# Kernel tuning notes

Hardware: AMD Instinct MI355X
Metric: run time of the kernel (lower is better)

The kernel has to match this reference:

```python
import jax, jax.numpy as jnp
import numpy as np

H = 32
W = 32
HIDDEN = 64
NUM_CLASSES = 10
BATCH = 128


def setup_inputs() -> dict:
    key = jax.random.key(0)
    ks = jax.random.split(key, 5)
    D = 4 * HIDDEN * H * W  # number_of_output_dimensions()
    return {
        "x": jax.random.normal(ks[0], (BATCH, 1, H, W), jnp.float32),
        "w_in": jax.random.normal(ks[1], (HIDDEN, 1), jnp.float32) * 0.1,
        "b_in": jnp.zeros((HIDDEN,), jnp.float32),
        "w_state": jax.random.normal(ks[2], (HIDDEN, HIDDEN, 2), jnp.float32) * (1.0 / np.sqrt(2 * HIDDEN)),
        "b_state": jnp.zeros((HIDDEN,), jnp.float32),
        "w_fc": jax.random.normal(ks[3], (D, NUM_CLASSES), jnp.float32) * 0.01,
        "b_fc": jnp.zeros((NUM_CLASSES,), jnp.float32),
    }


def _skew(x):
    # x: [B,1,H,W] -> [B,1,H,W+H-1]; row r shifted right by r (diagonal skew)
    Ws = W + H - 1
    col = jnp.arange(Ws)[None, :] - jnp.arange(H)[:, None]  # [H,Ws]
    valid = ((col >= 0) & (col < W)).astype(x.dtype)
    colc = jnp.clip(col, 0, W - 1)
    rows = jnp.arange(H)[:, None]
    return x[:, :, rows, colc] * valid[None, None]


def _one_direction(x, w_in, b_in, w_state, b_state):
    # Diagonal-scan MDRNN over skewed columns.
    B = x.shape[0]
    xs = _skew(x)  # [B,1,H,Ws]
    # Input projection for all columns at once (1x1 conv equivalent)
    xin = jnp.einsum('oc,bchw->bohw', w_in, xs) + b_in[None, :, None, None]
    cols = jnp.moveaxis(xin, 3, 0)  # [Ws,B,HIDDEN,H]

    w_up, w_same = w_state[:, :, 0], w_state[:, :, 1]

    def step(h, xc):
        # conv1d(kernel=2, padding=1) over column, bottom padding removed:
        # out[r] = w_up @ h[r-1] + w_same @ h[r]
        h_up = jnp.pad(h, ((0, 0), (0, 0), (1, 0)))[:, :, :H]
        s = (jnp.einsum('oi,bir->bor', w_up, h_up)
             + jnp.einsum('oi,bir->bor', w_same, h)
             + b_state[None, :, None])
        hn = jnp.tanh(s + xc)
        return hn, hn

    h0 = jnp.zeros((B, HIDDEN, H), x.dtype)
    _, ys = jax.lax.scan(step, h0, cols)  # [Ws,B,HIDDEN,H]
    acts = jnp.moveaxis(ys, 0, 3)  # [B,HIDDEN,H,Ws]
    # Unskew: out[..., r, c] = acts[..., r, c + r]
    ccols = jnp.arange(W)[None, :] + jnp.arange(H)[:, None]  # [H,W]
    rows = jnp.arange(H)[:, None]
    return acts[:, :, rows, ccols]  # [B,HIDDEN,H,W]


def reference(x, w_in, b_in, w_state, b_state, w_fc, b_fc):
    B = x.shape[0]
    # Four scanning directions via flips on dims 2 and 3, concatenated on batch
    x2 = x[:, :, ::-1, :]
    x3 = x[:, :, :, ::-1]
    x4 = x[:, :, ::-1, ::-1]
    xm = jnp.concatenate([x, x2, x3, x4], axis=0)  # [4B,1,H,W]
    acts = _one_direction(xm, w_in, b_in, w_state, b_state)  # [4B,HIDDEN,H,W]
    # index_select interleaving: example b gets its 4 direction copies contiguously
    sel = (jnp.arange(B)[:, None] + B * jnp.arange(4)[None, :]).reshape(-1)
    a = acts[sel].reshape(B, -1)  # [B, 4*HIDDEN*H*W]
    logits = a @ w_fc + b_fc
    return jax.nn.log_softmax(logits, axis=-1)
```

## Files before the change

### kernel.cpp

```cpp
#include <hip/hip_runtime.h>
#include <hip/hip_bf16.h>

#define NHID 64
#define NT   63
#define NBD  512
#define HLDS_STR 72
#define XSTR 35

typedef __attribute__((ext_vector_type(8))) short bf16x8;
typedef __attribute__((ext_vector_type(4))) float f32x4;

__device__ __forceinline__ float tanh_fast(float x) {
    const float e = __expf(2.0f * x);
    const float r = __builtin_amdgcn_rcpf(e + 1.0f);
    return 1.0f - 2.0f * r;
}

__device__ __forceinline__ unsigned int cvt_pk_bf16(float lo, float hi) {
    unsigned int r;
    asm("v_cvt_pk_bf16_f32 %0, %1, %2" : "=v"(r) : "v"(lo), "v"(hi));
    return r;
}

__device__ __forceinline__ float bf2f(unsigned int u16) {
    return __uint_as_float(u16 << 16);
}

#define SKEW_R0(t)  ((t) > 31 ? (t) - 31 : 0)
#define SKEW_R1(t)  ((t) < 31 ? (t) : 31)
#define SKEW_OFF(t) ((t) < 32 ? ((t) * ((t) + 1)) >> 1 : 1024 - (((63 - (t)) * (64 - (t))) >> 1))

#define LGKM_BARRIER() do {                                   \
    asm volatile("s_waitcnt lgkmcnt(0)" ::: "memory");        \
    __builtin_amdgcn_s_barrier();                             \
    asm volatile("" ::: "memory");                            \
} while (0)

__global__ __launch_bounds__(256, 2) void k_main(
    const float* __restrict__ x,
    const float* __restrict__ w_in,
    const float* __restrict__ b_in,
    const float* __restrict__ w_state,
    const float* __restrict__ b_state,
    unsigned short* __restrict__ acts_c,
    const float* __restrict__ w_fc,
    unsigned short* __restrict__ wt_swz)
{
    __shared__ __align__(16) unsigned short hA0[33 * HLDS_STR];
    __shared__ __align__(16) unsigned short hA1[33 * HLDS_STR];
    __shared__ __align__(16) unsigned short hB0[33 * HLDS_STR];
    __shared__ __align__(16) unsigned short hB1[33 * HLDS_STR];
    __shared__ float xsA[32 * XSTR];
    __shared__ float xsB[32 * XSTR];

    const int tid = threadIdx.x;

    if (blockIdx.x >= 256) {
        const int rel = blockIdx.x - 256;
        const int t   = rel >> 6;
        const int sub = rel & 63;
        const int r0 = SKEW_R0(t), r1 = SKEW_R1(t);
        const int cnt = r1 - r0 + 1;
        const int span = cnt << 10;
        int f = sub * 2048 + tid * 8;
        const int fdst = f;
        if (f >= 4 * span) return;
        int d = 0;
        while (f >= span) { f -= span; ++d; }
        const int ks   = f >> 9;
        const int lane = (f >> 3) & 63;
        const int g = lane >> 4, n = lane & 15;
        unsigned int pk[4];
        #pragma unroll
        for (int jj = 0; jj < 4; ++jj) {
            float v[2] = {0.0f, 0.0f};
            #pragma unroll
            for (int h = 0; h < 2; ++h) {
                const int j = jj * 2 + h;
                const int k = ks * 32 + g * 8 + j;
                const int r = r0 + (k >> 6);
                const int o = k & 63;
                const int c = t - r;
                if (n < 10)
                    v[h] = w_fc[((((size_t)(d * 64 + o)) << 10) + (r << 5) + c) * 10 + n];
            }
            pk[jj] = cvt_pk_bf16(v[0], v[1]);
        }
        uint4 st; st.x = pk[0]; st.y = pk[1]; st.z = pk[2]; st.w = pk[3];
        *(uint4*)(wt_swz + (size_t)SKEW_OFF(t) * 4096 + fdst) = st;
        return;
    }

    const int blk = blockIdx.x;
    const int bdA = 2 * blk;
    const int bdB = 2 * blk + 1;
    const int d   = bdA >> 7;
    const int bA  = bdA & 127;
    const int lane = tid & 63;
    const int wave = tid >> 6;
    const int wp = wave & 1;
    const int nt = wave >> 1;
    const int n  = lane & 15;
    const int g  = lane >> 4;

    const bool flr = (d & 1) != 0;
    const bool flc = (d & 2) != 0;
    const float* xbA = x + (size_t)bA * 1024;
    for (int idx = tid; idx < 1024; idx += 256) {
        const int r = idx >> 5, c = idx & 31;
        const int src = (flr ? 31 - r : r) * 32 + (flc ? 31 - c : c);
        xsA[r * XSTR + c] = xbA[src];
        xsB[r * XSTR + c] = xbA[1024 + src];
    }

    for (int m2 = tid; m2 < (33 * HLDS_STR) / 2; m2 += 256) {
        ((unsigned int*)hA0)[m2] = 0u;
        ((unsigned int*)hA1)[m2] = 0u;
        ((unsigned int*)hB0)[m2] = 0u;
        ((unsigned int*)hB1)[m2] = 0u;
    }

    bf16x8 a0[4], a1[4];
    #pragma unroll
    for (int wl = 0; wl < 2; ++wl) {
        const int o = wp * 32 + wl * 16 + n;
        #pragma unroll
        for (int kt = 0; kt < 4; ++kt) {
            const int s  = kt >> 1;
            const int cb = (kt & 1) * 32 + g * 8;
            bf16x8 w8;
            #pragma unroll
            for (int j = 0; j < 8; ++j) {
                const float w = w_state[((size_t)o * 64 + cb + j) * 2 + s];
                w8[j] = (short)(cvt_pk_bf16(w, 0.0f) & 0xffffu);
            }
            if (wl == 0) a0[kt] = w8; else a1[kt] = w8;
        }
    }

    float biasr[2][4], winr[2][4];
    #pragma unroll
    for (int wl = 0; wl < 2; ++wl)
        #pragma unroll
        for (int j = 0; j < 4; ++j) {
            const int o = wp * 32 + wl * 16 + g * 4 + j;
            biasr[wl][j] = b_in[o] + b_state[o];
            winr[wl][j]  = w_in[o];
        }

    const int r_out = nt * 16 + n;
    const int rdoff = r_out * HLDS_STR + g * 8;
    const int wroff = (r_out + 1) * HLDS_STR;
    const int cb0 = wp * 32 + g * 4;
    const int tlo = nt * 16;
    const float* xsA_r = &xsA[r_out * XSTR];
    const float* xsB_r = &xsB[r_out * XSTR];

    unsigned short* actpA = acts_c + (size_t)bdA * 65536 + (size_t)r_out * 1984 + cb0;
    unsigned short* actpB = acts_c + (size_t)bdB * 65536 + (size_t)r_out * 1984 + cb0;

    __syncthreads();

#define MFMA(F, B, C) C = __builtin_amdgcn_mfma_f32_16x16x32_bf16(F, B, C, 0, 0, 0)
#define EPI(WL, SA, SB, XV, WBUF, ACTP) {                                        \
    const float h0 = tanh_fast(SA[0] + SB[0] + biasr[WL][0] + winr[WL][0] * (XV)); \
    const float h1 = tanh_fast(SA[1] + SB[1] + biasr[WL][1] + winr[WL][1] * (XV)); \
    const float h2 = tanh_fast(SA[2] + SB[2] + biasr[WL][2] + winr[WL][2] * (XV)); \
    const float h3 = tanh_fast(SA[3] + SB[3] + biasr[WL][3] + winr[WL][3] * (XV)); \
    uint2 pk; pk.x = cvt_pk_bf16(h0, h1); pk.y = cvt_pk_bf16(h2, h3);            \
    *(uint2*)&WBUF[wroff + cb0 + (WL) * 16] = pk;                                \
    if (stv) *(uint2*)((ACTP) + (WL) * 16) = pk;                                 \
}

#define STEP(T, RA_, WA_, RB_, WB_) do {                                         \
    if ((unsigned)((T) - tlo) < 48u) {                                           \
        const bf16x8 fA0 = *(const bf16x8*)&RA_[rdoff];                          \
        const bf16x8 fA1 = *(const bf16x8*)&RA_[rdoff + 32];                     \
        const bf16x8 fA2 = *(const bf16x8*)&RA_[rdoff + HLDS_STR];               \
        const bf16x8 fA3 = *(const bf16x8*)&RA_[rdoff + HLDS_STR + 32];          \
        const bf16x8 fB0 = *(const bf16x8*)&RB_[rdoff];                          \
        const bf16x8 fB1 = *(const bf16x8*)&RB_[rdoff + 32];                     \
        const bf16x8 fB2 = *(const bf16x8*)&RB_[rdoff + HLDS_STR];               \
        const bf16x8 fB3 = *(const bf16x8*)&RB_[rdoff + HLDS_STR + 32];          \
        f32x4 sA0a = {0,0,0,0}, sA0b = {0,0,0,0};                                \
        f32x4 sA1a = {0,0,0,0}, sA1b = {0,0,0,0};                                \
        f32x4 sB0a = {0,0,0,0}, sB0b = {0,0,0,0};                                \
        f32x4 sB1a = {0,0,0,0}, sB1b = {0,0,0,0};                                \
        MFMA(a0[0], fA0, sA0a); MFMA(a1[0], fA0, sA1a);                          \
        MFMA(a0[0], fB0, sB0a); MFMA(a1[0], fB0, sB1a);                          \
        MFMA(a0[2], fA2, sA0b); MFMA(a1[2], fA2, sA1b);                          \
        MFMA(a0[2], fB2, sB0b); MFMA(a1[2], fB2, sB1b);                          \
        MFMA(a0[1], fA1, sA0a); MFMA(a1[1], fA1, sA1a);                          \
        MFMA(a0[1], fB1, sB0a); MFMA(a1[1], fB1, sB1a);                          \
        MFMA(a0[3], fA3, sA0b); MFMA(a1[3], fA3, sA1b);                          \
        MFMA(a0[3], fB3, sB0b); MFMA(a1[3], fB3, sB1b);                          \
        const int c_ = (T) - r_out;                                              \
        const bool stv = (unsigned)c_ < 32u;                                     \
        const float xvA = stv ? xsA_r[c_ & 31] : 0.0f;                           \
        const float xvB = stv ? xsB_r[c_ & 31] : 0.0f;                           \
        EPI(0, sA0a, sA0b, xvA, WA_, actpA); EPI(1, sA1a, sA1b, xvA, WA_, actpA);\
        EPI(0, sB0a, sB0b, xvB, WB_, actpB); EPI(1, sB1a, sB1b, xvB, WB_, actpB);\
    }                                                                            \
    LGKM_BARRIER();                                                              \
    actpA += 64; actpB += 64;                                                    \
} while (0)

    for (int sp = 0; sp < 31; ++sp) {
        const int t = 2 * sp;
        STEP(t,     hA0, hA1, hB0, hB1);
        STEP(t + 1, hA1, hA0, hB1, hB0);
    }
    STEP(62, hA0, hA1, hB0, hB1);
#undef STEP
#undef EPI
#undef MFMA
}

__global__ __launch_bounds__(256, 4) void k_fc(
    const unsigned short* __restrict__ acts_c,
    const unsigned short* __restrict__ wt_swz,
    float* __restrict__ partial)
{
    const int tid = threadIdx.x;
    const int blk = blockIdx.x;
    const int t   = blk >> 3;
    const int d   = (blk >> 1) & 3;
    const int mh  = blk & 1;
    const int lane = tid & 63;
    const int wv  = tid >> 6;
    const int g   = lane >> 4;
    const int n   = lane & 15;

    const int r0 = SKEW_R0(t), r1 = SKEW_R1(t);
    const int cnt = r1 - r0 + 1;
    const int off = SKEW_OFF(t);

    const int tb = d * 128 + mh * 64 + wv * 16;
    const unsigned short* Ap = acts_c + (size_t)(tb + n) * 65536
                             + (size_t)r0 * 1984 + (size_t)t * 64 + g * 8;
    const unsigned short* Bp = wt_swz
        + ((size_t)off * 4 + (size_t)d * cnt) * 1024 + lane * 8;

    f32x4 acc = {0.f, 0.f, 0.f, 0.f};
    #pragma unroll 2
    for (int q = 0; q < cnt; ++q) {
        const bf16x8 a0  = *(const bf16x8*)(Ap);
        const bf16x8 bb0 = *(const bf16x8*)(Bp);
        const bf16x8 a1  = *(const bf16x8*)(Ap + 32);
        const bf16x8 bb1 = *(const bf16x8*)(Bp + 512);
        acc = __builtin_amdgcn_mfma_f32_16x16x32_bf16(a0, bb0, acc, 0, 0, 0);
        acc = __builtin_amdgcn_mfma_f32_16x16x32_bf16(a1, bb1, acc, 0, 0, 0);
        Ap += 1984;
        Bp += 1024;
    }
    const int batch = tb + g * 4;
    #pragma unroll
    for (int reg = 0; reg < 4; ++reg)
        partial[((size_t)t * 512 + batch + reg) * 16 + n] = acc[reg];
}

__global__ __launch_bounds__(256) void k_out(
    const float* __restrict__ partial,
    const float* __restrict__ b_fc,
    float* __restrict__ out)
{
    __shared__ float lred[252 * 10];
    __shared__ float lgs[10];
    __shared__ float lse;
    const int b = blockIdx.x;
    const int tid = threadIdx.x;
    if (tid < 252) {
        const int t = tid >> 2, d = tid & 3;
        const float* p = partial + ((size_t)t * 512 + d * 128 + b) * 16;
        #pragma unroll
        for (int n2 = 0; n2 < 10; ++n2) lred[tid * 10 + n2] = p[n2];
    }
    __syncthreads();
    if (tid < 10) {
        float s = b_fc[tid];
        for (int i = 0; i < 252; ++i) s += lred[i * 10 + tid];
        lgs[tid] = s;
    }
    __syncthreads();
    if (tid == 0) {
        float m = lgs[0];
        for (int nn = 1; nn < 10; ++nn) m = fmaxf(m, lgs[nn]);
        float ssum = 0.0f;
        for (int nn = 0; nn < 10; ++nn) ssum += __expf(lgs[nn] - m);
        lse = m + __logf(ssum);
    }
    __syncthreads();
    if (tid < 10) out[b * 10 + tid] = lgs[tid] - lse;
}

extern "C" void kernel_launch(void* const* d_in, const int* in_sizes, int n_in,
                              void* d_out, int out_size, void* d_ws, size_t ws_size,
                              hipStream_t stream)
{
    const float* x       = (const float*)d_in[0];
    const float* w_in    = (const float*)d_in[1];
    const float* b_in    = (const float*)d_in[2];
    const float* w_state = (const float*)d_in[3];
    const float* b_state = (const float*)d_in[4];
    const float* w_fc    = (const float*)d_in[5];
    const float* b_fc    = (const float*)d_in[6];
    float* out = (float*)d_out;

    unsigned short* wt_swz = (unsigned short*)d_ws;
    float* partial = (float*)((char*)d_ws + (size_t)(8u << 20));
    unsigned short* acts_c = (unsigned short*)((char*)d_ws + (size_t)(16u << 20));

    k_main<<<4288, 256, 0, stream>>>(x, w_in, b_in, w_state, b_state,
                                     acts_c, w_fc, wt_swz);
    k_fc  <<<504, 256, 0, stream>>>(acts_c, wt_swz, partial);
    k_out <<<128, 256, 0, stream>>>(partial, b_fc, out);
}
```

Measured before the change: 76.93 us.

## Split recurrent scan over eight waves per block with 16 output channels each

Doubles the k_main block to 512 threads so each wave owns 16 output channels instead of 32, halving the MFMA and tanh work per wave on the serial 63-step diagonal scan. The w_fc swizzle blocks are regrouped to match the larger block size. k_fc also gets a higher occupancy hint and deeper unrolling. The cost is more waves meeting at each per-step barrier and more register or LDS pressure from 512-thread blocks at two blocks per CU.

```diff
diff --git a/kernel.cpp b/kernel.cpp
--- a/kernel.cpp
+++ b/kernel.cpp
@@ -22,10 +22,6 @@
     return r;
 }
 
-__device__ __forceinline__ float bf2f(unsigned int u16) {
-    return __uint_as_float(u16 << 16);
-}
-
 #define SKEW_R0(t)  ((t) > 31 ? (t) - 31 : 0)
 #define SKEW_R1(t)  ((t) < 31 ? (t) : 31)
 #define SKEW_OFF(t) ((t) < 32 ? ((t) * ((t) + 1)) >> 1 : 1024 - (((63 - (t)) * (64 - (t))) >> 1))
@@ -36,7 +32,7 @@
     asm volatile("" ::: "memory");                            \
 } while (0)
 
-__global__ __launch_bounds__(256, 2) void k_main(
+__global__ __launch_bounds__(512, 2) void k_main(
     const float* __restrict__ x,
     const float* __restrict__ w_in,
     const float* __restrict__ b_in,
@@ -57,12 +53,12 @@
 
     if (blockIdx.x >= 256) {
         const int rel = blockIdx.x - 256;
-        const int t   = rel >> 6;
-        const int sub = rel & 63;
+        const int t   = rel >> 5;
+        const int sub = rel & 31;
         const int r0 = SKEW_R0(t), r1 = SKEW_R1(t);
         const int cnt = r1 - r0 + 1;
         const int span = cnt << 10;
-        int f = sub * 2048 + tid * 8;
+        int f = sub * 4096 + tid * 8;
         const int fdst = f;
         if (f >= 4 * span) return;
         int d = 0;
@@ -98,32 +94,31 @@
     const int bA  = bdA & 127;
     const int lane = tid & 63;
     const int wave = tid >> 6;
-    const int wp = wave & 1;
-    const int nt = wave >> 1;
+    const int wo = wave >> 1;
+    const int wr = wave & 1;
     const int n  = lane & 15;
     const int g  = lane >> 4;
 
     const bool flr = (d & 1) != 0;
     const bool flc = (d & 2) != 0;
     const float* xbA = x + (size_t)bA * 1024;
-    for (int idx = tid; idx < 1024; idx += 256) {
+    for (int idx = tid; idx < 1024; idx += 512) {
         const int r = idx >> 5, c = idx & 31;
         const int src = (flr ? 31 - r : r) * 32 + (flc ? 31 - c : c);
         xsA[r * XSTR + c] = xbA[src];
         xsB[r * XSTR + c] = xbA[1024 + src];
     }
 
-    for (int m2 = tid; m2 < (33 * HLDS_STR) / 2; m2 += 256) {
+    for (int m2 = tid; m2 < (33 * HLDS_STR) / 2; m2 += 512) {
         ((unsigned int*)hA0)[m2] = 0u;
         ((unsigned int*)hA1)[m2] = 0u;
         ((unsigned int*)hB0)[m2] = 0u;
         ((unsigned int*)hB1)[m2] = 0u;
     }
 
-    bf16x8 a0[4], a1[4];
-    #pragma unroll
-    for (int wl = 0; wl < 2; ++wl) {
-        const int o = wp * 32 + wl * 16 + n;
+    bf16x8 a[4];
+    {
+        const int o = wo * 16 + n;
         #pragma unroll
         for (int kt = 0; kt < 4; ++kt) {
             const int s  = kt >> 1;
@@ -134,25 +129,23 @@
                 const float w = w_state[((size_t)o * 64 + cb + j) * 2 + s];
                 w8[j] = (short)(cvt_pk_bf16(w, 0.0f) & 0xffffu);
             }
-            if (wl == 0) a0[kt] = w8; else a1[kt] = w8;
+            a[kt] = w8;
         }
     }
 
-    float biasr[2][4], winr[2][4];
+    float biasr[4], winr[4];
     #pragma unroll
-    for (int wl = 0; wl < 2; ++wl)
-        #pragma unroll
-        for (int j = 0; j < 4; ++j) {
-            const int o = wp * 32 + wl * 16 + g * 4 + j;
-            biasr[wl][j] = b_in[o] + b_state[o];
-            winr[wl][j]  = w_in[o];
-        }
-
-    const int r_out = nt * 16 + n;
+    for (int j = 0; j < 4; ++j) {
+        const int o = wo * 16 + g * 4 + j;
+        biasr[j] = b_in[o] + b_state[o];
+        winr[j]  = w_in[o];
+    }
+
+    const int r_out = wr * 16 + n;
     const int rdoff = r_out * HLDS_STR + g * 8;
-    const int wroff = (r_out + 1) * HLDS_STR;
-    const int cb0 = wp * 32 + g * 4;
-    const int tlo = nt * 16;
+    const int wroff = (r_out + 1) * HLDS_STR + wo * 16 + g * 4;
+    const int cb0 = wo * 16 + g * 4;
+    const int tlo = wr * 16;
     const float* xsA_r = &xsA[r_out * XSTR];
     const float* xsB_r = &xsB[r_out * XSTR];
 
@@ -162,15 +155,6 @@
     __syncthreads();
 
 #define MFMA(F, B, C) C = __builtin_amdgcn_mfma_f32_16x16x32_bf16(F, B, C, 0, 0, 0)
-#define EPI(WL, SA, SB, XV, WBUF, ACTP) {                                        \
-    const float h0 = tanh_fast(SA[0] + SB[0] + biasr[WL][0] + winr[WL][0] * (XV)); \
-    const float h1 = tanh_fast(SA[1] + SB[1] + biasr[WL][1] + winr[WL][1] * (XV)); \
-    const float h2 = tanh_fast(SA[2] + SB[2] + biasr[WL][2] + winr[WL][2] * (XV)); \
-    const float h3 = tanh_fast(SA[3] + SB[3] + biasr[WL][3] + winr[WL][3] * (XV)); \
-    uint2 pk; pk.x = cvt_pk_bf16(h0, h1); pk.y = cvt_pk_bf16(h2, h3);            \
-    *(uint2*)&WBUF[wroff + cb0 + (WL) * 16] = pk;                                \
-    if (stv) *(uint2*)((ACTP) + (WL) * 16) = pk;                                 \
-}
 
 #define STEP(T, RA_, WA_, RB_, WB_) do {                                         \
     if ((unsigned)((T) - tlo) < 48u) {                                           \
@@ -182,24 +166,34 @@
         const bf16x8 fB1 = *(const bf16x8*)&RB_[rdoff + 32];                     \
         const bf16x8 fB2 = *(const bf16x8*)&RB_[rdoff + HLDS_STR];               \
         const bf16x8 fB3 = *(const bf16x8*)&RB_[rdoff + HLDS_STR + 32];          \
-        f32x4 sA0a = {0,0,0,0}, sA0b = {0,0,0,0};                                \
-        f32x4 sA1a = {0,0,0,0}, sA1b = {0,0,0,0};                                \
-        f32x4 sB0a = {0,0,0,0}, sB0b = {0,0,0,0};                                \
-        f32x4 sB1a = {0,0,0,0}, sB1b = {0,0,0,0};                                \
-        MFMA(a0[0], fA0, sA0a); MFMA(a1[0], fA0, sA1a);                          \
-        MFMA(a0[0], fB0, sB0a); MFMA(a1[0], fB0, sB1a);                          \
-        MFMA(a0[2], fA2, sA0b); MFMA(a1[2], fA2, sA1b);                          \
-        MFMA(a0[2], fB2, sB0b); MFMA(a1[2], fB2, sB1b);                          \
-        MFMA(a0[1], fA1, sA0a); MFMA(a1[1], fA1, sA1a);                          \
-        MFMA(a0[1], fB1, sB0a); MFMA(a1[1], fB1, sB1a);                          \
-        MFMA(a0[3], fA3, sA0b); MFMA(a1[3], fA3, sA1b);                          \
-        MFMA(a0[3], fB3, sB0b); MFMA(a1[3], fB3, sB1b);                          \
+        f32x4 sAa = {0,0,0,0}, sAb = {0,0,0,0};                                  \
+        f32x4 sBa = {0,0,0,0}, sBb = {0,0,0,0};                                  \
+        MFMA(a[0], fA0, sAa); MFMA(a[0], fB0, sBa);                              \
+        MFMA(a[2], fA2, sAb); MFMA(a[2], fB2, sBb);                              \
+        MFMA(a[1], fA1, sAa); MFMA(a[1], fB1, sBa);                              \
+        MFMA(a[3], fA3, sAb); MFMA(a[3], fB3, sBb);                              \
         const int c_ = (T) - r_out;                                              \
         const bool stv = (unsigned)c_ < 32u;                                     \
         const float xvA = stv ? xsA_r[c_ & 31] : 0.0f;                           \
         const float xvB = stv ? xsB_r[c_ & 31] : 0.0f;                           \
-        EPI(0, sA0a, sA0b, xvA, WA_, actpA); EPI(1, sA1a, sA1b, xvA, WA_, actpA);\
-        EPI(0, sB0a, sB0b, xvB, WB_, actpB); EPI(1, sB1a, sB1b, xvB, WB_, actpB);\
+        {                                                                        \
+            const float h0 = tanh_fast(sAa[0] + sAb[0] + biasr[0] + winr[0] * xvA); \
+            const float h1 = tanh_fast(sAa[1] + sAb[1] + biasr[1] + winr[1] * xvA); \
+            const float h2 = tanh_fast(sAa[2] + sAb[2] + biasr[2] + winr[2] * xvA); \
+            const float h3 = tanh_fast(sAa[3] + sAb[3] + biasr[3] + winr[3] * xvA); \
+            uint2 pk; pk.x = cvt_pk_bf16(h0, h1); pk.y = cvt_pk_bf16(h2, h3);    \
+            *(uint2*)&WA_[wroff] = pk;                                           \
+            if (stv) *(uint2*)(actpA) = pk;                                      \
+        }                                                                        \
+        {                                                                        \
+            const float h0 = tanh_fast(sBa[0] + sBb[0] + biasr[0] + winr[0] * xvB); \
+            const float h1 = tanh_fast(sBa[1] + sBb[1] + biasr[1] + winr[1] * xvB); \
+            const float h2 = tanh_fast(sBa[2] + sBb[2] + biasr[2] + winr[2] * xvB); \
+            const float h3 = tanh_fast(sBa[3] + sBb[3] + biasr[3] + winr[3] * xvB); \
+            uint2 pk; pk.x = cvt_pk_bf16(h0, h1); pk.y = cvt_pk_bf16(h2, h3);    \
+            *(uint2*)&WB_[wroff] = pk;                                           \
+            if (stv) *(uint2*)(actpB) = pk;                                      \
+        }                                                                        \
     }                                                                            \
     LGKM_BARRIER();                                                              \
     actpA += 64; actpB += 64;                                                    \
@@ -212,11 +206,10 @@
     }
     STEP(62, hA0, hA1, hB0, hB1);
 #undef STEP
-#undef EPI
 #undef MFMA
 }
 
-__global__ __launch_bounds__(256, 4) void k_fc(
+__global__ __launch_bounds__(256, 8) void k_fc(
     const unsigned short* __restrict__ acts_c,
     const unsigned short* __restrict__ wt_swz,
     float* __restrict__ partial)
@@ -242,7 +235,7 @@
         + ((size_t)off * 4 + (size_t)d * cnt) * 1024 + lane * 8;
 
     f32x4 acc = {0.f, 0.f, 0.f, 0.f};
-    #pragma unroll 2
+    #pragma unroll 4
     for (int q = 0; q < cnt; ++q) {
         const bf16x8 a0  = *(const bf16x8*)(Ap);
         const bf16x8 bb0 = *(const bf16x8*)(Bp);
@@ -310,7 +303,7 @@
     float* partial = (float*)((char*)d_ws + (size_t)(8u << 20));
     unsigned short* acts_c = (unsigned short*)((char*)d_ws + (size_t)(16u << 20));
 
-    k_main<<<4288, 256, 0, stream>>>(x, w_in, b_in, w_state, b_state,
+    k_main<<<2272, 512, 0, stream>>>(x, w_in, b_in, w_state, b_state,
                                      acts_c, w_fc, wt_swz);
     k_fc  <<<504, 256, 0, stream>>>(acts_c, wt_swz, partial);
     k_out <<<128, 256, 0, stream>>>(partial, b_fc, out);
```

Result: faster. 71.13 us (-7.5%).
